# Kernel optimization log

Measured on AMD Instinct MI355X. Metric: run time of the kernel, lower is better.

The kernel has to match this reference:

```python
import jax, jax.numpy as jnp
import numpy as np
import math

BZ, SEQ, NV, VA, HA = 16, 5, 1, 8, 8
C, DSTATE, DCONV, EXPAND, NLAYER = 384, 16, 4, 2, 4
DI = EXPAND * C
DTR = math.ceil(C / 16)  # 24
NTOK = (NV + 2) * SEQ * VA * HA  # 960 multi-modal tokens
T = NTOK + 2                     # + 2 gps tokens


def _ln(x, g, b, eps=1e-5):
    m = jnp.mean(x, -1, keepdims=True)
    v = jnp.mean((x - m) ** 2, -1, keepdims=True)
    return (x - m) * jax.lax.rsqrt(v + eps) * g + b


def _mamba(x, in_w, cw, cb, xw, dtw, dtb, a_log, d, ow):
    # x: (B,T,C); Mamba with bias=False in/out proj, conv_bias=True (mamba_ssm defaults)
    xz = jnp.einsum('btc,ec->bte', x, in_w)            # (B,T,2*DI)
    xh, z = jnp.split(xz, 2, axis=-1)
    xt = jnp.swapaxes(xh, 1, 2)                        # (B,DI,T)
    xt = jax.lax.conv_general_dilated(
        xt, cw[:, None, :], (1,), [(DCONV - 1, 0)],
        feature_group_count=DI, dimension_numbers=('NCH', 'OIH', 'NCH'))
    xh = jax.nn.silu(jnp.swapaxes(xt, 1, 2) + cb)      # causal depthwise conv + SiLU
    xdbl = jnp.einsum('btd,ed->bte', xh, xw)           # (B,T,DTR+2*DS)
    dt, Bm, Cm = jnp.split(xdbl, [DTR, DTR + DSTATE], axis=-1)
    dt = jax.nn.softplus(jnp.einsum('btr,dr->btd', dt, dtw) + dtb)  # (B,T,DI)
    A = -jnp.exp(a_log)                                # (DI,DSTATE)

    def step(h, inp):
        dt_t, x_t, b_t, c_t = inp                      # (B,DI),(B,DI),(B,DS),(B,DS)
        h = h * jnp.exp(dt_t[..., None] * A) + (dt_t * x_t)[..., None] * b_t[:, None, :]
        return h, jnp.einsum('bds,bs->bd', h, c_t)

    h0 = jnp.zeros((x.shape[0], DI, DSTATE), x.dtype)
    xs = tuple(jnp.swapaxes(a, 0, 1) for a in (dt, xh, Bm, Cm))
    _, ys = jax.lax.scan(step, h0, xs)
    y = jnp.swapaxes(ys, 0, 1) + d * xh
    y = y * jax.nn.silu(z)
    return jnp.einsum('btd,cd->btc', y, ow)


def _forward(image_tensor, lidar_tensor, radar_tensor, gps, pos_emb,
             ln1_g, ln1_b, fc1_w, fc1_b, fc2_w, fc2_b,
             in_proj_w, conv_w, conv_b, x_proj_w, dt_proj_w, dt_proj_b,
             A_log, D_param, out_proj_w, ln_f_g, ln_f_b):
    bz = lidar_tensor.shape[0] // SEQ
    h, w = lidar_tensor.shape[2], lidar_tensor.shape[3]
    img = image_tensor.reshape(bz, NV * SEQ, -1, h, w)
    lid = lidar_tensor.reshape(bz, SEQ, -1, h, w)
    rad = radar_tensor.reshape(bz, SEQ, -1, h, w)
    s1, s2 = C // 3, C // 3 * 2
    cs_img = jnp.concatenate([img[:, :, :s1], lid[:, :, s1:s2], rad[:, :, s2:]], axis=2)
    cs_lid = jnp.concatenate([lid[:, :, :s1], rad[:, :, s1:s2], img[:, :, s2:]], axis=2)
    cs_rad = jnp.concatenate([rad[:, :, :s1], img[:, :, s1:s2], lid[:, :, s2:]], axis=2)
    tok = jnp.concatenate([cs_img, cs_lid, cs_rad], axis=1)     # (bz, 3*SEQ, C, h, w)
    tok = jnp.transpose(tok, (0, 1, 3, 4, 2)).reshape(bz, -1, C)
    tok = jnp.concatenate([tok, gps], axis=1)                   # (bz, T, C)
    x = pos_emb + tok                                           # dropout is identity (eval)
    for l in range(NLAYER):
        x_ln = _ln(x, ln1_g[l], ln1_b[l])
        x_fc1 = jnp.einsum('btc,ec->bte', x_ln, fc1_w[l]) + fc1_b[l]
        x_fm = _mamba(x_fc1, in_proj_w[l, 0], conv_w[l, 0], conv_b[l, 0],
                      x_proj_w[l, 0], dt_proj_w[l, 0], dt_proj_b[l, 0],
                      A_log[l, 0], D_param[l, 0], out_proj_w[l, 0])
        x_flip = jnp.flip(x_fc1, axis=1)
        x_bm = _mamba(x_flip, in_proj_w[l, 1], conv_w[l, 1], conv_b[l, 1],
                      x_proj_w[l, 1], dt_proj_w[l, 1], dt_proj_b[l, 1],
                      A_log[l, 1], D_param[l, 1], out_proj_w[l, 1])
        x_fc2 = jnp.einsum('btc,ec->bte', x_flip, fc2_w[l]) + fc2_b[l]
        x_relu = jnp.where(x_fc2 >= 0, x_fc2, 0.2 * x_fc2)      # LeakyReLU(0.2)
        x = x_bm * x_relu + x_fm * x_bm                         # note: x_bm stays flipped, as in original
    x = _ln(x, ln_f_g, ln_f_b)
    pos_out = x[:, NTOK:]
    x = x[:, :NTOK].reshape(bz, (NV + 2) * SEQ, VA, HA, C)
    x = jnp.transpose(x, (0, 1, 4, 2, 3))
    img_out = x[:, :NV * SEQ].reshape(bz * NV * SEQ, -1, h, w)
    lid_out = x[:, NV * SEQ:(NV + 1) * SEQ].reshape(bz * SEQ, -1, h, w)
    rad_out = x[:, (NV + 1) * SEQ:].reshape(bz * SEQ, -1, h, w)
    return img_out, lid_out, rad_out, pos_out


def setup_inputs() -> dict:
    key = jax.random.key(0)
    it = iter(jax.random.split(key, 24))

    def n(shape, s=0.02):
        return jax.random.normal(next(it), shape, jnp.float32) * s

    return dict(
        image_tensor=n((BZ * NV * SEQ, C, VA, HA), 1.0),
        lidar_tensor=n((BZ * SEQ, C, VA, HA), 1.0),
        radar_tensor=n((BZ * SEQ, C, VA, HA), 1.0),
        gps=n((BZ, 2, C), 1.0),
        pos_emb=n((1, T, C), 0.02),
        ln1_g=jnp.ones((NLAYER, C)), ln1_b=jnp.zeros((NLAYER, C)),
        fc1_w=n((NLAYER, C, C)), fc1_b=jnp.zeros((NLAYER, C)),
        fc2_w=n((NLAYER, C, C)), fc2_b=jnp.zeros((NLAYER, C)),
        in_proj_w=n((NLAYER, 2, 2 * DI, C)),
        conv_w=n((NLAYER, 2, DI, DCONV), 0.1),
        conv_b=jnp.zeros((NLAYER, 2, DI)),
        x_proj_w=n((NLAYER, 2, DTR + 2 * DSTATE, DI)),
        dt_proj_w=n((NLAYER, 2, DI, DTR), 0.1),
        dt_proj_b=jnp.full((NLAYER, 2, DI), -4.6, jnp.float32),  # softplus ~ 0.01
        A_log=jnp.tile(jnp.log(jnp.arange(1., DSTATE + 1, dtype=jnp.float32)), (NLAYER, 2, DI, 1)),
        D_param=jnp.ones((NLAYER, 2, DI)),
        out_proj_w=n((NLAYER, 2, C, DI)),
        ln_f_g=jnp.ones((C,)), ln_f_b=jnp.zeros((C,)),
    )


def reference(image_tensor, lidar_tensor, radar_tensor, gps, pos_emb,
              ln1_g, ln1_b, fc1_w, fc1_b, fc2_w, fc2_b,
              in_proj_w, conv_w, conv_b, x_proj_w, dt_proj_w, dt_proj_b,
              A_log, D_param, out_proj_w, ln_f_g, ln_f_b):
    return _forward(image_tensor, lidar_tensor, radar_tensor, gps, pos_emb,
                    ln1_g, ln1_b, fc1_w, fc1_b, fc2_w, fc2_b,
                    in_proj_w, conv_w, conv_b, x_proj_w, dt_proj_w, dt_proj_b,
                    A_log, D_param, out_proj_w, ln_f_g, ln_f_b)
```

## Files before the change

### kernel.cpp

```cpp
#include <hip/hip_runtime.h>
#include <cstdint>
#include <cstddef>


constexpr int BZv = 16, SEQ = 5, NV = 1;
constexpr int C = 384, DSTATE = 16, DCONV = 4, NLAYER = 4;
constexpr int DI = 768;
constexpr int DTR = 24;
constexpr int NTOK = (NV + 2) * SEQ * 64;
constexpr int T = NTOK + 2;
constexpr int M = BZv * T;
constexpr int HB = 8;
constexpr int MH = HB * T;
constexpr int XZdim = 2 * DI;
constexpr int ND = DTR + 2 * DSTATE;
constexpr int NDP = 32;
constexpr int NCHUNK = 13, TC = 74;
constexpr int NQ = 241;
constexpr size_t SEC_SZ = (size_t)BZv * SEQ * C * 64;

constexpr size_t SET1 = (size_t)C * C;
constexpr size_t SETI = (size_t)2 * DI * C;
constexpr size_t SETO = (size_t)C * DI;
constexpr size_t SETX = (size_t)64 * DI;
constexpr size_t SETD = (size_t)DI * 32;
constexpr size_t WSZ1 = 4 * SET1;
constexpr size_t WSZI = 8 * SETI;
constexpr size_t WSZO = 8 * SETO;
constexpr size_t WSZX = 8 * SETX;
constexpr size_t WSZD = 8 * SETD;

typedef __attribute__((ext_vector_type(8))) short short8;
typedef __attribute__((ext_vector_type(4))) float floatx4;

#define GLOAD_LDS16(g, l)                                        \
  __builtin_amdgcn_global_load_lds(                              \
      (const __attribute__((address_space(1))) void*)(g),        \
      (__attribute__((address_space(3))) void*)(l), 16, 0, 0)

__device__ __forceinline__ void split_bf16(float v, short& hi, short& lo) {
  unsigned u = __float_as_uint(v);
  unsigned hib = u & 0xFFFF0000u;
  float r = v - __uint_as_float(hib);
  hi = (short)(hib >> 16);
  lo = (short)(__float_as_uint(r) >> 16);
}

__device__ __forceinline__ float join_bf16(short h, short l) {
  return __uint_as_float((unsigned)(unsigned short)h << 16) +
         __uint_as_float((unsigned)(unsigned short)l << 16);
}

__device__ __forceinline__ void pow16(float e1, float* e) {
  e[0] = e1;
  e[1] = e1 * e1;
  e[3] = e[1] * e[1];
  e[7] = e[3] * e[3];
  e[15] = e[7] * e[7];
  e[2] = e[1] * e[0];
  e[4] = e[3] * e[0];
  e[5] = e[3] * e[1];
  e[6] = e[5] * e[0];
  e[8] = e[7] * e[0];
  e[9] = e[7] * e[1];
  e[10] = e[9] * e[0];
  e[11] = e[7] * e[3];
  e[12] = e[11] * e[0];
  e[13] = e[11] * e[1];
  e[14] = e[13] * e[0];
}

__global__ __launch_bounds__(256) void assemble_t_k(
    const float* __restrict__ img, const float* __restrict__ lid,
    const float* __restrict__ rad, const float* __restrict__ gps,
    const float* __restrict__ pe, float* __restrict__ x) {
  __shared__ float lds[64][129];
  int blk = blockIdx.x, tid = threadIdx.x;
  if (blk < 720) {
    int b = blk / 45;
    int rem = blk % 45;
    int g_ = rem / 3, cc = rem % 3;
    int sec = g_ / 5, s = g_ % 5;
    int srow = b * 5 + s;
    int which = (cc + sec) % 3;
    const float* src = (which == 0) ? img : (which == 1 ? lid : rad);
    const float* sp = src + (size_t)srow * (C * 64) + cc * 8192;
#pragma unroll
    for (int i = 0; i < 32; i++) {
      int lin = tid + 256 * i;
      lds[lin & 63][lin >> 6] = sp[lin];
    }
    __syncthreads();
#pragma unroll
    for (int i = 0; i < 32; i++) {
      int lin = tid + 256 * i;
      int p = lin >> 7, c = lin & 127;
      int t = g_ * 64 + p;
      int ccc = cc * 128 + c;
      x[((size_t)b * T + t) * C + ccc] = lds[p][c] + pe[(size_t)t * C + ccc];
    }
  } else {
#pragma unroll
    for (int i = 0; i < 48; i++) {
      int lin = tid + 256 * i;
      int r = lin / C, c = lin % C;
      int b = r >> 1, e = r & 1;
      x[((size_t)b * T + NTOK + e) * C + c] =
          gps[((size_t)b * 2 + e) * C + c] + pe[(size_t)(NTOK + e) * C + c];
    }
  }
}

__global__ __launch_bounds__(256) void ln_fused_k(
    const float* __restrict__ x, const float* __restrict__ g,
    const float* __restrict__ b, short* __restrict__ oh,
    short* __restrict__ ol) {
  int row = blockIdx.x * 4 + (threadIdx.x >> 6);
  int lane = threadIdx.x & 63;
  const float* xr = x + (size_t)row * C;
  float v[6];
  float s = 0.f;
#pragma unroll
  for (int j = 0; j < 6; j++) {
    v[j] = xr[lane + 64 * j];
    s += v[j];
  }
#pragma unroll
  for (int o = 32; o > 0; o >>= 1) s += __shfl_xor(s, o, 64);
  float mean = s * (1.f / 384.f);
  float q = 0.f;
#pragma unroll
  for (int j = 0; j < 6; j++) {
    float d = v[j] - mean;
    q += d * d;
  }
#pragma unroll
  for (int o = 32; o > 0; o >>= 1) q += __shfl_xor(q, o, 64);
  float rstd = rsqrtf(q * (1.f / 384.f) + 1e-5f);
#pragma unroll
  for (int j = 0; j < 6; j++) {
    int c = lane + 64 * j;
    float val = (v[j] - mean) * rstd * g[c] + b[c];
    short h, l;
    split_bf16(val, h, l);
    oh[(size_t)row * C + c] = h;
    ol[(size_t)row * C + c] = l;
  }
}

__global__ __launch_bounds__(256) void ln_stats2_k(const float* __restrict__ x,
                                                   float* __restrict__ stats) {
  int row = blockIdx.x * 4 + (threadIdx.x >> 6);
  int lane = threadIdx.x & 63;
  const float* xr = x + (size_t)row * C;
  float v[6];
  float s = 0.f;
#pragma unroll
  for (int j = 0; j < 6; j++) {
    v[j] = xr[lane + 64 * j];
    s += v[j];
  }
#pragma unroll
  for (int o = 32; o > 0; o >>= 1) s += __shfl_xor(s, o, 64);
  float mean = s * (1.f / 384.f);
  float q = 0.f;
#pragma unroll
  for (int j = 0; j < 6; j++) {
    float d = v[j] - mean;
    q += d * d;
  }
#pragma unroll
  for (int o = 32; o > 0; o >>= 1) q += __shfl_xor(q, o, 64);
  if (lane == 0) {
    stats[2 * row] = mean;
    stats[2 * row + 1] = rsqrtf(q * (1.f / 384.f) + 1e-5f);
  }
}

template <int NSRC, int KSRC, int KS>
__global__ __launch_bounds__(256) void cast_swz_k(const float* __restrict__ src,
                                                  short* __restrict__ oh,
                                                  short* __restrict__ ol) {
  constexpr int NP = (NSRC + 15) & ~15;
  constexpr size_t SETSZ = (size_t)NP * KS * 32;
  int set = blockIdx.y;
  size_t idx = (size_t)blockIdx.x * 256 + threadIdx.x;
  int e = (int)(idx & 7);
  int lane = (int)((idx >> 3) & 63);
  size_t rest = idx >> 9;
  int ks = (int)(rest % KS);
  int nf = (int)(rest / KS);
  int n = nf * 16 + (lane & 15);
  int k = ks * 32 + ((lane >> 4) << 3) + e;
  float v = 0.f;
  if (n < NSRC && k < KSRC)
    v = src[(size_t)set * NSRC * KSRC + (size_t)n * KSRC + k];
  short h, l;
  split_bf16(v, h, l);
  oh[(size_t)set * SETSZ + idx] = h;
  ol[(size_t)set * SETSZ + idx] = l;
}

template <int ACT, bool BIAS, bool FLIPA, bool OSPLIT, bool SWAPXY>
__global__ __launch_bounds__(256) void mgemm_k(
    const short* __restrict__ Ah, const short* __restrict__ Al, int K,
    const short* __restrict__ Wh, const short* __restrict__ Wl, int N,
    const float* __restrict__ bias, float* __restrict__ Co, int ldc,
    short* __restrict__ Oh, short* __restrict__ Ol, int Mrows, int arow_off,
    int crow_off) {
  __shared__ __align__(16) short sAh[128 * 32];
  __shared__ __align__(16) short sAl[128 * 32];
  const int tid = threadIdx.x;
  const int wave = tid >> 6, lane = tid & 63;
  const int bm_ = SWAPXY ? blockIdx.x : blockIdx.y;
  const int bn_ = SWAPXY ? blockIdx.y : blockIdx.x;
  const int m0 = bm_ * 128, n0 = bn_ * 128;
  const int lrow = lane >> 2, lchunk = lane & 3;
  const int wm = (wave >> 1) * 64, wn = (wave & 1) * 64;
  const int frow = lane & 15, fquad = lane >> 4;
  const int KST = K >> 5;
  const int nfb = (n0 + wn) >> 4;

  size_t arow[2];
#pragma unroll
  for (int p = 0; p < 2; p++) {
    int r = p * 64 + wave * 16 + lrow;
    int lm = m0 + r;
    if (lm >= Mrows) lm = Mrows - 1;
    int g = arow_off + lm;
    if (FLIPA) {
      int bb = g / T;
      int tt = g - bb * T;
      g = bb * T + (T - 1 - tt);
    }
    arow[p] = (size_t)g * K;
  }

  floatx4 acc[4][4] = {};
  for (int k0 = 0; k0 < K; k0 += 32) {
    if (k0) __syncthreads();
    const int kc = k0 + lchunk * 8;
#pragma unroll
    for (int p = 0; p < 2; p++) {
      GLOAD_LDS16(Ah + arow[p] + kc, &sAh[(p * 64 + wave * 16) * 32]);
      GLOAD_LDS16(Al + arow[p] + kc, &sAl[(p * 64 + wave * 16) * 32]);
    }
    const int ks = k0 >> 5;
    short8 bh[4], bl[4];
#pragma unroll
    for (int j = 0; j < 4; j++) {
      size_t bo = (((size_t)(nfb + j) * KST + ks) * 64 + lane) * 8;
      bh[j] = *(const short8*)&Wh[bo];
      bl[j] = *(const short8*)&Wl[bo];
    }
    __syncthreads();
    short8 ah[4], al[4];
#pragma unroll
    for (int i = 0; i < 4; i++) {
      int ra = (wm + i * 16 + frow) * 32 + fquad * 8;
      ah[i] = *(const short8*)&sAh[ra];
      al[i] = *(const short8*)&sAl[ra];
    }
#pragma unroll
    for (int i = 0; i < 4; i++)
#pragma unroll
      for (int j = 0; j < 4; j++) {
        acc[i][j] = __builtin_amdgcn_mfma_f32_16x16x32_bf16(ah[i], bh[j],
                                                            acc[i][j], 0, 0, 0);
        acc[i][j] = __builtin_amdgcn_mfma_f32_16x16x32_bf16(al[i], bh[j],
                                                            acc[i][j], 0, 0, 0);
        acc[i][j] = __builtin_amdgcn_mfma_f32_16x16x32_bf16(ah[i], bl[j],
                                                            acc[i][j], 0, 0, 0);
      }
  }
#pragma unroll
  for (int i = 0; i < 4; i++) {
#pragma unroll
    for (int r = 0; r < 4; r++) {
      int gm = m0 + wm + i * 16 + fquad * 4 + r;
      if (gm >= Mrows) continue;
      int grow = crow_off + gm;
#pragma unroll
      for (int j = 0; j < 4; j++) {
        int gn = n0 + wn + j * 16 + frow;
        if (gn >= N) continue;
        float v = acc[i][j][r];
        if constexpr (BIAS) v += bias[gn];
        if constexpr (ACT == 1) v = v >= 0.f ? v : 0.2f * v;
        if constexpr (OSPLIT) {
          short h, l;
          split_bf16(v, h, l);
          Oh[(size_t)grow * N + gn] = h;
          Ol[(size_t)grow * N + gn] = l;
        } else {
          Co[(size_t)grow * ldc + gn] = v;
        }
      }
    }
  }
}

template <int ACT, bool BIAS, int OMODE>
__global__ __launch_bounds__(256) void mgemm64_k(
    const short* __restrict__ Ah, const short* __restrict__ Al, int lda, int K,
    const short* __restrict__ Wh, const short* __restrict__ Wl, int N,
    const float* __restrict__ bias, float* __restrict__ Co, int ldc,
    short* __restrict__ Oh, short* __restrict__ Ol,
    const float* __restrict__ e1, const float* __restrict__ e2, int Mrows,
    int crow_off) {
  __shared__ __align__(16) short sAh[64 * 32];
  __shared__ __align__(16) short sAl[64 * 32];
  const int tid = threadIdx.x;
  const int wave = tid >> 6, lane = tid & 63;
  const int m0 = blockIdx.y * 64, n0 = blockIdx.x * 64;
  const int schunk = tid & 3;
  const int frow = lane & 15, fquad = lane >> 4;
  const int KST = K >> 5;
  const int nfw = (n0 >> 4) + wave;

  int lm = m0 + (tid >> 2);
  if (lm >= Mrows) lm = Mrows - 1;
  size_t aoff = (size_t)lm * lda;

  floatx4 acc[4] = {};
  for (int k0 = 0; k0 < K; k0 += 32) {
    if (k0) __syncthreads();
    const int kc = k0 + schunk * 8;
    GLOAD_LDS16(Ah + aoff + kc, &sAh[(wave * 16) * 32]);
    GLOAD_LDS16(Al + aoff + kc, &sAl[(wave * 16) * 32]);
    const int ks = k0 >> 5;
    short8 bh, bl;
    {
      size_t bo = (((size_t)nfw * KST + ks) * 64 + lane) * 8;
      bh = *(const short8*)&Wh[bo];
      bl = *(const short8*)&Wl[bo];
    }
    __syncthreads();
    short8 ah[4], al[4];
#pragma unroll
    for (int i = 0; i < 4; i++) {
      int ra = (i * 16 + frow) * 32 + fquad * 8;
      ah[i] = *(const short8*)&sAh[ra];
      al[i] = *(const short8*)&sAl[ra];
    }
#pragma unroll
    for (int i = 0; i < 4; i++) {
      acc[i] = __builtin_amdgcn_mfma_f32_16x16x32_bf16(ah[i], bh, acc[i], 0, 0, 0);
      acc[i] = __builtin_amdgcn_mfma_f32_16x16x32_bf16(al[i], bh, acc[i], 0, 0, 0);
      acc[i] = __builtin_amdgcn_mfma_f32_16x16x32_bf16(ah[i], bl, acc[i], 0, 0, 0);
    }
  }
  const int gn = n0 + wave * 16 + frow;
  if (gn < N) {
#pragma unroll
    for (int i = 0; i < 4; i++) {
#pragma unroll
      for (int r = 0; r < 4; r++) {
        int gm = m0 + i * 16 + fquad * 4 + r;
        if (gm >= Mrows) continue;
        int grow = crow_off + gm;
        float v = acc[i][r];
        if constexpr (BIAS) v += bias[gn];
        if constexpr (ACT == 2) v = (v > 20.f) ? v : __logf(1.f + __expf(v));
        if constexpr (ACT == 4) {
          size_t o = (size_t)grow * ldc + gn;
          v = e2[o] * (e1[o] + v);
        }
        if constexpr (OMODE == 2) {
          if (gn < NDP) {
            short h, l;
            split_bf16(v, h, l);
            Oh[(size_t)grow * NDP + gn] = h;
            Ol[(size_t)grow * NDP + gn] = l;
          }
          if (gn >= DTR) Co[(size_t)grow * 32 + (gn - DTR)] = v;
        } else {
          Co[(size_t)grow * ldc + gn] = v;
        }
      }
    }
  }
}

__global__ __launch_bounds__(256) void conv_k(const float* __restrict__ xz,
                                              const float* __restrict__ cw,
                                              const float* __restrict__ cb,
                                              short* __restrict__ xch,
                                              short* __restrict__ xcl) {
  int idx = blockIdx.x * 256 + threadIdx.x;
  int dh = idx % (DI / 2);
  int rem = idx / (DI / 2);
  int q = rem % NQ;
  int b = rem / NQ;
  int d = dh * 2;
  int t0 = q * 4;
  const float* base = xz + (size_t)b * T * XZdim + d;
  float4 cwa = *(const float4*)&cw[d * 4];
  float4 cwb = *(const float4*)&cw[(d + 1) * 4];
  float cb0 = cb[d], cb1 = cb[d + 1];
  float2 w[7];
#pragma unroll
  for (int j = 0; j < 7; j++) {
    int tt = t0 - 3 + j;
    w[j] = (tt >= 0 && tt < T) ? *(const float2*)(base + (size_t)tt * XZdim)
                               : make_float2(0.f, 0.f);
  }
  const float cwx[4] = {cwa.x, cwa.y, cwa.z, cwa.w};
  const float cwy[4] = {cwb.x, cwb.y, cwb.z, cwb.w};
#pragma unroll
  for (int r = 0; r < 4; r++) {
    int t = t0 + r;
    if (t >= T) break;
    float a0 = cb0, a1 = cb1;
#pragma unroll
    for (int j = 0; j < 4; j++) {
      a0 += w[r + j].x * cwx[j];
      a1 += w[r + j].y * cwy[j];
    }
    float v0 = a0 / (1.f + __expf(-a0));
    float v1 = a1 / (1.f + __expf(-a1));
    short h0, l0, h1, l1;
    split_bf16(v0, h0, l0);
    split_bf16(v1, h1, l1);
    size_t o = ((size_t)b * T + t) * DI + d;
    *(short2*)&xch[o] = make_short2(h0, h1);
    *(short2*)&xcl[o] = make_short2(l0, l1);
  }
}

__global__ __launch_bounds__(256) void scan_p1_k(
    const float* __restrict__ xzb, const short* __restrict__ xch,
    const short* __restrict__ xcl, const float* __restrict__ xdbc,
    const float* __restrict__ alog, float* __restrict__ hchk,
    float* __restrict__ sdt) {
  int d = blockIdx.x * 256 + threadIdx.x;
  int ch = blockIdx.y, b = blockIdx.z;
  float A[DSTATE], h[DSTATE];
  bool powA = true;
#pragma unroll
  for (int s = 0; s < DSTATE; s++) {
    A[s] = -expf(alog[d * DSTATE + s]);
    powA = powA && (fabsf(A[s] + (float)(s + 1)) <= 1e-4f * (float)(s + 1));
    h[s] = 0.f;
  }
  const int t0 = ch * TC;
  const float* xzr = xzb + ((size_t)b * T + t0) * XZdim;
  const short* xchr = xch + ((size_t)b * T + t0) * DI;
  const short* xclr = xcl + ((size_t)b * T + t0) * DI;
  const float* bcr = xdbc + ((size_t)b * T + t0) * 32;
  float sd = 0.f;
  if (powA) {
    for (int t = 0; t < TC; t++) {
      float dt = xzr[(size_t)t * XZdim + d];
      float xv = join_bf16(xchr[(size_t)t * DI + d], xclr[(size_t)t * DI + d]);
      float dx = dt * xv;
      const float* bc = bcr + (size_t)t * 32;
      sd += dt;
      float ev[DSTATE];
      pow16(__expf(-dt), ev);
#pragma unroll
      for (int s = 0; s < DSTATE; s++) h[s] = h[s] * ev[s] + dx * bc[s];
    }
  } else {
    for (int t = 0; t < TC; t++) {
      float dt = xzr[(size_t)t * XZdim + d];
      float xv = join_bf16(xchr[(size_t)t * DI + d], xclr[(size_t)t * DI + d]);
      float dx = dt * xv;
      const float* bc = bcr + (size_t)t * 32;
      sd += dt;
#pragma unroll
      for (int s = 0; s < DSTATE; s++)
        h[s] = h[s] * __expf(dt * A[s]) + dx * bc[s];
    }
  }
  size_t o = ((size_t)(b * NCHUNK + ch) * DSTATE) * DI + d;
#pragma unroll
  for (int s = 0; s < DSTATE; s++) hchk[o + (size_t)s * DI] = h[s];
  sdt[(size_t)(b * NCHUNK + ch) * DI + d] = sd;
}

__global__ __launch_bounds__(256) void scan_p2_k(float* __restrict__ hchk,
                                                 const float* __restrict__ sdt,
                                                 const float* __restrict__ alog) {
  int idx = blockIdx.x * 256 + threadIdx.x;
  int d = idx % DI;
  int rem = idx / DI;
  int s = rem % DSTATE, b = rem / DSTATE;
  float A = -expf(alog[d * DSTATE + s]);
  float hin = 0.f;
#pragma unroll
  for (int ch = 0; ch < NCHUNK; ch++) {
    size_t o = ((size_t)(b * NCHUNK + ch) * DSTATE + s) * DI + d;
    float P = __expf(A * sdt[(size_t)(b * NCHUNK + ch) * DI + d]);
    float hl = hchk[o];
    hchk[o] = hin;
    hin = P * hin + hl;
  }
}

__global__ __launch_bounds__(256) void scan_p3_k(
    const float* __restrict__ xzb, const short* __restrict__ xch,
    const short* __restrict__ xcl, const float* __restrict__ xdbc,
    const float* __restrict__ alog, const float* __restrict__ Dp,
    const float* __restrict__ hchk, short* __restrict__ yh,
    short* __restrict__ yl) {
  int d = blockIdx.x * 256 + threadIdx.x;
  int ch = blockIdx.y, b = blockIdx.z;
  float A[DSTATE], h[DSTATE];
  bool powA = true;
  size_t o = ((size_t)(b * NCHUNK + ch) * DSTATE) * DI + d;
#pragma unroll
  for (int s = 0; s < DSTATE; s++) {
    A[s] = -expf(alog[d * DSTATE + s]);
    powA = powA && (fabsf(A[s] + (float)(s + 1)) <= 1e-4f * (float)(s + 1));
    h[s] = hchk[o + (size_t)s * DI];
  }
  float Dd = Dp[d];
  const int t0 = ch * TC;
  const float* xzr = xzb + ((size_t)b * T + t0) * XZdim;
  const short* xchr = xch + ((size_t)b * T + t0) * DI;
  const short* xclr = xcl + ((size_t)b * T + t0) * DI;
  const float* bcr = xdbc + ((size_t)b * T + t0) * 32;
  if (powA) {
    for (int t = 0; t < TC; t++) {
      float dt = xzr[(size_t)t * XZdim + d];
      float xv = join_bf16(xchr[(size_t)t * DI + d], xclr[(size_t)t * DI + d]);
      float zv = xzr[(size_t)t * XZdim + DI + d];
      float dx = dt * xv;
      float accv = 0.f;
      const float* bc = bcr + (size_t)t * 32;
      float ev[DSTATE];
      pow16(__expf(-dt), ev);
#pragma unroll
      for (int s = 0; s < DSTATE; s++) {
        h[s] = h[s] * ev[s] + dx * bc[s];
        accv += h[s] * bc[DSTATE + s];
      }
      float y = accv + Dd * xv;
      float sz = zv / (1.f + __expf(-zv));
      float v = y * sz;
      short hh, ll;
      split_bf16(v, hh, ll);
      size_t oi = ((size_t)(b * T + t0 + t)) * DI + d;
      yh[oi] = hh;
      yl[oi] = ll;
    }
  } else {
    for (int t = 0; t < TC; t++) {
      float dt = xzr[(size_t)t * XZdim + d];
      float xv = join_bf16(xchr[(size_t)t * DI + d], xclr[(size_t)t * DI + d]);
      float zv = xzr[(size_t)t * XZdim + DI + d];
      float dx = dt * xv;
      float accv = 0.f;
      const float* bc = bcr + (size_t)t * 32;
#pragma unroll
      for (int s = 0; s < DSTATE; s++) {
        h[s] = h[s] * __expf(dt * A[s]) + dx * bc[s];
        accv += h[s] * bc[DSTATE + s];
      }
      float y = accv + Dd * xv;
      float sz = zv / (1.f + __expf(-zv));
      float v = y * sz;
      short hh, ll;
      split_bf16(v, hh, ll);
      size_t oi = ((size_t)(b * T + t0 + t)) * DI + d;
      yh[oi] = hh;
      yl[oi] = ll;
    }
  }
}

__global__ __launch_bounds__(256) void ln_scatter_k(
    const float* __restrict__ x, const float* __restrict__ stats,
    const float* __restrict__ g, const float* __restrict__ bb,
    float* __restrict__ out) {
  __shared__ float lds[64][129];
  int blk = blockIdx.x, tid = threadIdx.x;
  if (blk < 240) {
    int b = blk / 15, g_ = blk % 15;
    int sec = g_ / 5, s = g_ % 5;
    const int rbase = b * T + g_ * 64;
    for (int cc = 0; cc < 3; cc++) {
      if (cc) __syncthreads();
#pragma unroll
      for (int i = 0; i < 32; i++) {
        int lin = tid + 256 * i;
        int p = lin >> 7, c = lin & 127;
        int row = rbase + p;
        int ccc = cc * 128 + c;
        float v = x[(size_t)row * C + ccc];
        v = (v - stats[2 * row]) * stats[2 * row + 1] * g[ccc] + bb[ccc];
        lds[p][c] = v;
      }
      __syncthreads();
      size_t obase = (size_t)sec * SEC_SZ +
                     (((size_t)(b * 5 + s) * C + cc * 128) << 6);
#pragma unroll
      for (int i = 0; i < 32; i++) {
        int lin = tid + 256 * i;
        int c = lin >> 6, p = lin & 63;
        out[obase + ((size_t)c << 6) + p] = lds[p][c];
      }
    }
  } else {
#pragma unroll
    for (int i = 0; i < 48; i++) {
      int lin = tid + 256 * i;
      int r = lin / C, c = lin % C;
      int b = r >> 1, e = r & 1;
      int row = b * T + NTOK + e;
      float v = x[(size_t)row * C + c];
      v = (v - stats[2 * row]) * stats[2 * row + 1] * g[c] + bb[c];
      out[3 * SEC_SZ + ((size_t)(b * 2 + e)) * C + c] = v;
    }
  }
}

extern "C" void kernel_launch(void* const* d_in, const int* in_sizes, int n_in,
                              void* d_out, int out_size, void* d_ws,
                              size_t ws_size, hipStream_t stream) {
  const float* image = (const float*)d_in[0];
  const float* lidar = (const float*)d_in[1];
  const float* radar = (const float*)d_in[2];
  const float* gps = (const float*)d_in[3];
  const float* pe = (const float*)d_in[4];
  const float* ln1g = (const float*)d_in[5];
  const float* ln1b = (const float*)d_in[6];
  const float* fc1w = (const float*)d_in[7];
  const float* fc1b = (const float*)d_in[8];
  const float* fc2w = (const float*)d_in[9];
  const float* fc2b_ = (const float*)d_in[10];
  const float* inw = (const float*)d_in[11];
  const float* cw = (const float*)d_in[12];
  const float* cb = (const float*)d_in[13];
  const float* xw = (const float*)d_in[14];
  const float* dtw = (const float*)d_in[15];
  const float* dtb = (const float*)d_in[16];
  const float* alog = (const float*)d_in[17];
  const float* Dp = (const float*)d_in[18];
  const float* ow = (const float*)d_in[19];
  const float* lnfg = (const float*)d_in[20];
  const float* lnfb = (const float*)d_in[21];
  float* out = (float*)d_out;

  constexpr size_t MC = (size_t)M * C;
  float* ws = (float*)d_ws;
  float* x = ws;
  float* fcb = x + MC;
  float* bmfm = fcb + MC;
  float* x1f = bmfm + MC;
  float* yf = x1f + MC;
  float* xz_h = yf + MC;
  float* xcp = xz_h + (size_t)MH * XZdim;
  float* xdp = xcp + (size_t)MH * DI;
  constexpr size_t CHK_H = (size_t)HB * NCHUNK * DSTATE * DI;
  float* hchk = xdp + (size_t)MH * 64;
  float* sdtb = hchk + CHK_H;
  float* wpl = sdtb + (size_t)HB * NCHUNK * DI;
  float* stats2 = hchk;

  short* lnh = (short*)bmfm;
  short* lnl = lnh + MC;
  float* bm = bmfm;
  short* x1h = (short*)x1f;
  short* x1l = x1h + MC;
  short* yh = (short*)yf;
  short* yl = yh + (size_t)MH * DI;
  short* xch = (short*)xcp;
  short* xcl = xch + (size_t)MH * DI;
  short* xdh = (short*)xdp;
  short* xdl = xdh + (size_t)MH * NDP;
  float* xdbc = xdp + (size_t)MH * 32;

  short* wf1h = (short*)wpl;
  short* wf1l = wf1h + WSZ1;
  short* wf2h = wf1l + WSZ1;
  short* wf2l = wf2h + WSZ1;
  short* winh = wf2l + WSZ1;
  short* winl = winh + WSZI;
  short* wowh = winl + WSZI;
  short* wowl = wowh + WSZO;
  short* wxh = wowl + WSZO;
  short* wxl = wxh + WSZX;
  short* wdth = wxl + WSZX;
  short* wdtl = wdth + WSZD;

  cast_swz_k<C, C, 12><<<dim3((int)(SET1 / 256), 4), 256, 0, stream>>>(
      fc1w, wf1h, wf1l);
  cast_swz_k<C, C, 12><<<dim3((int)(SET1 / 256), 4), 256, 0, stream>>>(
      fc2w, wf2h, wf2l);
  cast_swz_k<2 * DI, C, 12><<<dim3((int)(SETI / 256), 8), 256, 0, stream>>>(
      inw, winh, winl);
  cast_swz_k<C, DI, 24><<<dim3((int)(SETO / 256), 8), 256, 0, stream>>>(
      ow, wowh, wowl);
  cast_swz_k<ND, DI, 24><<<dim3((int)(SETX / 256), 8), 256, 0, stream>>>(
      xw, wxh, wxl);
  cast_swz_k<DI, DTR, 1><<<dim3((int)(SETD / 256), 8), 256, 0, stream>>>(
      dtw, wdth, wdtl);

  assemble_t_k<<<721, 256, 0, stream>>>(image, lidar, radar, gps, pe, x);

  for (int l = 0; l < NLAYER; l++) {
    ln_fused_k<<<M / 4, 256, 0, stream>>>(x, ln1g + l * C, ln1b + l * C, lnh,
                                          lnl);
    mgemm_k<0, true, false, true, false><<<dim3(3, 121), 256, 0, stream>>>(
        lnh, lnl, C, wf1h + l * SET1, wf1l + l * SET1, C, fc1b + l * C,
        nullptr, 0, x1h, x1l, M, 0, 0);
    mgemm_k<1, true, true, false, false><<<dim3(3, 121), 256, 0, stream>>>(
        x1h, x1l, C, wf2h + l * SET1, wf2l + l * SET1, C, fc2b_ + l * C, fcb,
        C, nullptr, nullptr, M, 0, 0);
    for (int di = 0; di < 2; di++) {
      const int dir = 1 - di;
      size_t wo = (size_t)(l * 2 + dir);
      for (int h = 0; h < 2; h++) {
        const int roff = h * MH;
        if (dir == 0)
          mgemm_k<0, false, false, false, true><<<dim3(61, 12), 256, 0, stream>>>(
              x1h, x1l, C, winh + wo * SETI, winl + wo * SETI, 2 * DI, nullptr,
              xz_h, XZdim, nullptr, nullptr, MH, roff, 0);
        else
          mgemm_k<0, false, true, false, true><<<dim3(61, 12), 256, 0, stream>>>(
              x1h, x1l, C, winh + wo * SETI, winl + wo * SETI, 2 * DI, nullptr,
              xz_h, XZdim, nullptr, nullptr, MH, roff, 0);
        conv_k<<<(HB * NQ * (DI / 2)) / 256, 256, 0, stream>>>(
            xz_h, cw + wo * DI * DCONV, cb + wo * DI, xch, xcl);
        mgemm64_k<0, false, 2><<<dim3(1, 121), 256, 0, stream>>>(
            xch, xcl, DI, DI, wxh + wo * SETX, wxl + wo * SETX, ND, nullptr,
            xdbc, 0, xdh, xdl, nullptr, nullptr, MH, 0);
        mgemm64_k<2, true, 0><<<dim3(12, 121), 256, 0, stream>>>(
            xdh, xdl, NDP, 32, wdth + wo * SETD, wdtl + wo * SETD, DI,
            dtb + wo * DI, xz_h, XZdim, nullptr, nullptr, nullptr, nullptr,
            MH, 0);
        scan_p1_k<<<dim3(3, NCHUNK, HB), 256, 0, stream>>>(
            xz_h, xch, xcl, xdbc, alog + wo * DI * DSTATE, hchk, sdtb);
        scan_p2_k<<<(HB * DSTATE * DI) / 256, 256, 0, stream>>>(
            hchk, sdtb, alog + wo * DI * DSTATE);
        scan_p3_k<<<dim3(3, NCHUNK, HB), 256, 0, stream>>>(
            xz_h, xch, xcl, xdbc, alog + wo * DI * DSTATE, Dp + wo * DI, hchk,
            yh, yl);
        if (dir == 1)
          mgemm64_k<0, false, 0><<<dim3(6, 121), 256, 0, stream>>>(
              yh, yl, DI, DI, wowh + wo * SETO, wowl + wo * SETO, C, nullptr,
              bm, C, nullptr, nullptr, nullptr, nullptr, MH, roff);
        else
          mgemm64_k<4, false, 0><<<dim3(6, 121), 256, 0, stream>>>(
              yh, yl, DI, DI, wowh + wo * SETO, wowl + wo * SETO, C, nullptr,
              x, C, nullptr, nullptr, fcb, bm, MH, roff);
      }
    }
  }
  ln_stats2_k<<<M / 4, 256, 0, stream>>>(x, stats2);
  ln_scatter_k<<<241, 256, 0, stream>>>(x, stats2, lnfg, lnfb, out);
}
```

Baseline: 3.345 ms.

## Double scan chunk count and use 16-row tiles for x_proj GEMM

Doubles the number of scan chunks per sequence (26 chunks of 37 steps) so the chunked selective scan launches more blocks with shorter serial loops. The x_proj GEMM gets a 16-row M-tile variant, raising its grid from 121 to 481 blocks so more CUs are busy on this narrow-N GEMM. To fit the larger chunk-state buffers, hchk/sdtb are aliased into the upper half of the x buffer, and stats2 is moved past the weight area. The costs are more work in the inter-chunk pass, lower data reuse per GEMM block, and some risk from the buffer aliasing.

```diff
diff --git a/kernel.cpp b/kernel.cpp
--- a/kernel.cpp
+++ b/kernel.cpp
@@ -15,7 +15,7 @@
 constexpr int XZdim = 2 * DI;
 constexpr int ND = DTR + 2 * DSTATE;
 constexpr int NDP = 32;
-constexpr int NCHUNK = 13, TC = 74;
+constexpr int NCHUNK = 26, TC = 37;
 constexpr int NQ = 241;
 constexpr size_t SEC_SZ = (size_t)BZv * SEQ * C * 64;
 
@@ -300,7 +300,7 @@
   }
 }
 
-template <int ACT, bool BIAS, int OMODE>
+template <int ACT, bool BIAS, int OMODE, int MT = 64>
 __global__ __launch_bounds__(256) void mgemm64_k(
     const short* __restrict__ Ah, const short* __restrict__ Al, int lda, int K,
     const short* __restrict__ Wh, const short* __restrict__ Wl, int N,
@@ -308,26 +308,31 @@
     short* __restrict__ Oh, short* __restrict__ Ol,
     const float* __restrict__ e1, const float* __restrict__ e2, int Mrows,
     int crow_off) {
-  __shared__ __align__(16) short sAh[64 * 32];
-  __shared__ __align__(16) short sAl[64 * 32];
+  __shared__ __align__(16) short sAh[MT * 32];
+  __shared__ __align__(16) short sAl[MT * 32];
   const int tid = threadIdx.x;
   const int wave = tid >> 6, lane = tid & 63;
-  const int m0 = blockIdx.y * 64, n0 = blockIdx.x * 64;
+  const int m0 = blockIdx.y * MT, n0 = blockIdx.x * 64;
   const int schunk = tid & 3;
   const int frow = lane & 15, fquad = lane >> 4;
   const int KST = K >> 5;
   const int nfw = (n0 >> 4) + wave;
 
-  int lm = m0 + (tid >> 2);
+  int lm = m0 + ((MT == 64) ? (tid >> 2) : (lane >> 2));
   if (lm >= Mrows) lm = Mrows - 1;
   size_t aoff = (size_t)lm * lda;
 
-  floatx4 acc[4] = {};
+  floatx4 acc[MT / 16] = {};
   for (int k0 = 0; k0 < K; k0 += 32) {
     if (k0) __syncthreads();
     const int kc = k0 + schunk * 8;
-    GLOAD_LDS16(Ah + aoff + kc, &sAh[(wave * 16) * 32]);
-    GLOAD_LDS16(Al + aoff + kc, &sAl[(wave * 16) * 32]);
+    if constexpr (MT == 64) {
+      GLOAD_LDS16(Ah + aoff + kc, &sAh[(wave * 16) * 32]);
+      GLOAD_LDS16(Al + aoff + kc, &sAl[(wave * 16) * 32]);
+    } else {
+      if (wave == 0) GLOAD_LDS16(Ah + aoff + kc, &sAh[0]);
+      if (wave == 1) GLOAD_LDS16(Al + aoff + kc, &sAl[0]);
+    }
     const int ks = k0 >> 5;
     short8 bh, bl;
     {
@@ -336,15 +341,15 @@
       bl = *(const short8*)&Wl[bo];
     }
     __syncthreads();
-    short8 ah[4], al[4];
-#pragma unroll
-    for (int i = 0; i < 4; i++) {
+    short8 ah[MT / 16], al[MT / 16];
+#pragma unroll
+    for (int i = 0; i < MT / 16; i++) {
       int ra = (i * 16 + frow) * 32 + fquad * 8;
       ah[i] = *(const short8*)&sAh[ra];
       al[i] = *(const short8*)&sAl[ra];
     }
 #pragma unroll
-    for (int i = 0; i < 4; i++) {
+    for (int i = 0; i < MT / 16; i++) {
       acc[i] = __builtin_amdgcn_mfma_f32_16x16x32_bf16(ah[i], bh, acc[i], 0, 0, 0);
       acc[i] = __builtin_amdgcn_mfma_f32_16x16x32_bf16(al[i], bh, acc[i], 0, 0, 0);
       acc[i] = __builtin_amdgcn_mfma_f32_16x16x32_bf16(ah[i], bl, acc[i], 0, 0, 0);
@@ -353,7 +358,7 @@
   const int gn = n0 + wave * 16 + frow;
   if (gn < N) {
 #pragma unroll
-    for (int i = 0; i < 4; i++) {
+    for (int i = 0; i < MT / 16; i++) {
 #pragma unroll
       for (int r = 0; r < 4; r++) {
         int gm = m0 + i * 16 + fquad * 4 + r;
@@ -653,11 +658,12 @@
   float* xz_h = yf + MC;
   float* xcp = xz_h + (size_t)MH * XZdim;
   float* xdp = xcp + (size_t)MH * DI;
+  float* wpl = xdp + (size_t)MH * 64;
+
   constexpr size_t CHK_H = (size_t)HB * NCHUNK * DSTATE * DI;
-  float* hchk = xdp + (size_t)MH * 64;
+  static_assert(CHK_H + (size_t)HB * NCHUNK * DI <= MC / 2, "alias overflow");
+  float* hchk = x + MC / 2;
   float* sdtb = hchk + CHK_H;
-  float* wpl = sdtb + (size_t)HB * NCHUNK * DI;
-  float* stats2 = hchk;
 
   short* lnh = (short*)bmfm;
   short* lnl = lnh + MC;
@@ -684,6 +690,7 @@
   short* wxl = wxh + WSZX;
   short* wdth = wxl + WSZX;
   short* wdtl = wdth + WSZD;
+  float* stats2 = (float*)(wdtl + WSZD);
 
   cast_swz_k<C, C, 12><<<dim3((int)(SET1 / 256), 4), 256, 0, stream>>>(
       fc1w, wf1h, wf1l);
@@ -724,7 +731,7 @@
               xz_h, XZdim, nullptr, nullptr, MH, roff, 0);
         conv_k<<<(HB * NQ * (DI / 2)) / 256, 256, 0, stream>>>(
             xz_h, cw + wo * DI * DCONV, cb + wo * DI, xch, xcl);
-        mgemm64_k<0, false, 2><<<dim3(1, 121), 256, 0, stream>>>(
+        mgemm64_k<0, false, 2, 16><<<dim3(1, MH / 16), 256, 0, stream>>>(
             xch, xcl, DI, DI, wxh + wo * SETX, wxl + wo * SETX, ND, nullptr,
             xdbc, 0, xdh, xdl, nullptr, nullptr, MH, 0);
         mgemm64_k<2, true, 0><<<dim3(12, 121), 256, 0, stream>>>(
```

New measurement: 3.068 ms. -8.3%, faster.
